# Kernel tuning notes

Hardware: AMD Instinct MI355X
Metric: run time of the kernel (lower is better)

## Reference

```python
import jax, jax.numpy as jnp
import numpy as np

B, M, FIN, FOUT, K, E = 4, 50000, 128, 128, 4, 800000


def setup_inputs() -> dict:
    key = jax.random.key(0)
    ks = jax.random.split(key, 8)
    x = jax.random.normal(ks[0], (B, M, FIN), dtype=jnp.float32)
    L_rows = jax.random.randint(ks[1], (E,), 0, M, dtype=jnp.int32)
    L_cols = jax.random.randint(ks[2], (E,), 0, M, dtype=jnp.int32)
    # stands in for the rescaled (0.75 * (2L/lmax - I)) Laplacian values
    L_vals = jax.random.normal(ks[3], (E,), dtype=jnp.float32) * 0.05
    stddev = 1.0 / np.sqrt(FIN * (K + 0.5) / 2.0)
    kernel = jax.random.normal(ks[4], (K * FIN, FOUT), dtype=jnp.float32) * stddev
    W_down = jax.random.normal(ks[5], (FOUT, FOUT // 8), dtype=jnp.float32) * (1.0 / np.sqrt(FOUT))
    b_down = jnp.zeros((FOUT // 8,), dtype=jnp.float32)
    W_up = jax.random.normal(ks[6], (FOUT // 8, FOUT), dtype=jnp.float32) * (1.0 / np.sqrt(FOUT // 8))
    b_up = jnp.zeros((FOUT,), dtype=jnp.float32)
    return {"x": x, "L_vals": L_vals, "L_rows": L_rows, "L_cols": L_cols,
            "kernel": kernel, "W_down": W_down, "b_down": b_down,
            "W_up": W_up, "b_up": b_up}


def reference(x, L_vals, L_rows, L_cols, kernel, W_down, b_down, W_up, b_up):
    B_, M_, Fin = x.shape
    K_ = kernel.shape[0] // Fin

    def spmm(X):  # sparse L [M,M] @ dense X [M, D]
        return jax.ops.segment_sum(L_vals[:, None] * X[L_cols], L_rows, num_segments=M_)

    # Chebyshev recurrence, operating on [M, Fin*B] like the TF code
    x0 = x.transpose(1, 2, 0).reshape(M_, Fin * B_)
    stack = [x0]
    if K_ > 1:
        x1 = spmm(x0)
        stack.append(x1)
    for _ in range(2, K_):
        x2 = 2.0 * spmm(x1) - x0
        stack.append(x2)
        x0, x1 = x1, x2

    # [K,M,Fin*B] -> [K,M,Fin,B] -> [B,M,Fin,K] -> [B*M, Fin*K]
    xs = jnp.stack(stack, axis=0).reshape(K_, M_, Fin, B_)
    xs = xs.transpose(3, 1, 2, 0).reshape(B_ * M_, Fin * K_)
    y = (xs @ kernel).reshape(B_, M_, -1)
    y = jax.nn.relu(y)

    # SE block: avg-pool over nodes, down (swish), up (sigmoid), scale
    s = jnp.mean(y, axis=1, keepdims=True)          # [B, 1, Fout]
    d = jax.nn.swish(s @ W_down + b_down)           # [B, 1, Fout/8]
    u = jax.nn.sigmoid(d @ W_up + b_up)             # [B, 1, Fout]
    return y * u
```

## Files before the change

kernel.cpp:

```cpp
#include <hip/hip_runtime.h>
#include <hip/hip_bf16.h>

#define BB 4
#define MM 50000
#define FINF 128
#define FOUTF 128
#define KCH 4
#define EE 800000
#define NROWS (BB*MM)
#define XC 512
#define CD 512

__device__ __forceinline__ float bf2f(unsigned short u){
    union{unsigned int i; float f;} v; v.i = ((unsigned int)u) << 16; return v.f;
}
__device__ __forceinline__ unsigned short f2bf(float f){
    union{float f; unsigned int i;} v; v.f = f;
    unsigned int r = v.i + 0x7FFF + ((v.i >> 16) & 1);
    return (unsigned short)(r >> 16);
}

typedef __bf16 bf16x8 __attribute__((ext_vector_type(8)));
typedef float  f32x4  __attribute__((ext_vector_type(4)));

__global__ __launch_bounds__(256) void k_init_x0(const float* __restrict__ x,
                                                 unsigned short* __restrict__ X0){
    int tid = blockIdx.x*256 + threadIdx.x;
    if (tid >= BB*MM*FINF/4) return;
    int f4 = tid & 31;
    int t  = tid >> 5;
    int m  = t % MM, b = t / MM;
    float4 v = ((const float4*)x)[tid];
    ushort4 o;
    o.x = f2bf(v.x); o.y = f2bf(v.y); o.z = f2bf(v.z); o.w = f2bf(v.w);
    *(ushort4*)(X0 + (size_t)m*XC + b*FINF + f4*4) = o;
}

__global__ __launch_bounds__(256) void k_prepw(const float* __restrict__ kern,
                                               unsigned short* __restrict__ Wt){
    int tid = blockIdx.x*256 + threadIdx.x;
    int c = tid & 511, n = tid >> 9;
    int kc = c >> 7, f = c & 127;
    int ns = n >> 4, l16 = n & 15;
    int ks = c >> 5, rem = c & 31, g = rem >> 3, j = rem & 7;
    int lane = g*16 + l16;
    Wt[((ns*16 + ks)*64 + lane)*8 + j] = f2bf(kern[(f*KCH + kc)*FOUTF + n]);
}

__global__ __launch_bounds__(256) void k_hist(const int* __restrict__ rows, int* __restrict__ counts){
    int e = blockIdx.x*256 + threadIdx.x;
    if (e < EE) atomicAdd(&counts[rows[e]], 1);
}

__global__ __launch_bounds__(1024) void k_scan(const int* __restrict__ counts,
                                               int* __restrict__ offs, int* __restrict__ cursor){
    __shared__ int part[1024];
    const int CH = (MM + 1023) / 1024;
    int t = threadIdx.x;
    int lo = t*CH; if (lo > MM) lo = MM;
    int hi = lo + CH; if (hi > MM) hi = MM;
    int s = 0;
    for (int i = lo; i < hi; ++i) s += counts[i];
    part[t] = s; __syncthreads();
    for (int d = 1; d < 1024; d <<= 1){
        int v = (t >= d) ? part[t-d] : 0;
        __syncthreads();
        part[t] += v;
        __syncthreads();
    }
    int run = (t == 0) ? 0 : part[t-1];
    for (int i = lo; i < hi; ++i){
        offs[i] = run; cursor[i] = run; run += counts[i];
    }
    if (t == 1023) offs[MM] = part[1023];
}

__global__ __launch_bounds__(256) void k_scatter(const int* __restrict__ rows, const int* __restrict__ cols,
                                                 const float* __restrict__ vals, int* __restrict__ cursor,
                                                 int* __restrict__ colv, float* __restrict__ valv){
    int e = blockIdx.x*256 + threadIdx.x;
    if (e >= EE) return;
    int r = rows[e];
    int pos = atomicAdd(&cursor[r], 1);
    colv[pos] = cols[e]; valv[pos] = vals[e];
}

__global__ __launch_bounds__(128) void k_spmm(const unsigned short* __restrict__ Xin,
                                              const unsigned short* __restrict__ Xprev,
                                              unsigned short* __restrict__ Xout,
                                              const int* __restrict__ offs,
                                              const int* __restrict__ colv,
                                              const float* __restrict__ valv,
                                              float alpha, int sub){
    int m = blockIdx.x, t = threadIdx.x;
    int c0 = t*4;
    int start = offs[m], end = offs[m+1];
    float a0=0.f, a1=0.f, a2=0.f, a3=0.f;

    int n  = end - start;
    int nb = n & ~3;
    int burst_end = start + nb;
    int j = start;

    int   cc[4];
    float vv[4];
    if (j < burst_end){
        #pragma unroll
        for (int q = 0; q < 4; ++q){ cc[q] = colv[j+q]; vv[q] = valv[j+q]; }
    }
    while (j < burst_end){
        int   c_[4];
        float v_[4];
        #pragma unroll
        for (int q = 0; q < 4; ++q){ c_[q] = cc[q]; v_[q] = vv[q]; }
        j += 4;
        if (j < burst_end){
            #pragma unroll
            for (int q = 0; q < 4; ++q){ cc[q] = colv[j+q]; vv[q] = valv[j+q]; }
        }
        ushort4 xv[4];
        #pragma unroll
        for (int q = 0; q < 4; ++q)
            xv[q] = *(const ushort4*)(Xin + (size_t)c_[q]*XC + c0);
        #pragma unroll
        for (int q = 0; q < 4; ++q){
            a0 += v_[q]*bf2f(xv[q].x); a1 += v_[q]*bf2f(xv[q].y);
            a2 += v_[q]*bf2f(xv[q].z); a3 += v_[q]*bf2f(xv[q].w);
        }
    }
    for (; j < end; ++j){
        int col = colv[j]; float val = valv[j];
        ushort4 xv = *(const ushort4*)(Xin + (size_t)col*XC + c0);
        a0 += val*bf2f(xv.x); a1 += val*bf2f(xv.y);
        a2 += val*bf2f(xv.z); a3 += val*bf2f(xv.w);
    }

    a0 *= alpha; a1 *= alpha; a2 *= alpha; a3 *= alpha;
    if (sub){
        ushort4 pv = *(const ushort4*)(Xprev + (size_t)m*XC + c0);
        a0 -= bf2f(pv.x); a1 -= bf2f(pv.y); a2 -= bf2f(pv.z); a3 -= bf2f(pv.w);
    }
    ushort4 o; o.x = f2bf(a0); o.y = f2bf(a1); o.z = f2bf(a2); o.w = f2bf(a3);
    *(ushort4*)(Xout + (size_t)m*XC + c0) = o;
}

__global__ __launch_bounds__(256, 2) void k_gemm(const unsigned short* __restrict__ X0,
                                                 const unsigned short* __restrict__ X1,
                                                 const unsigned short* __restrict__ X2,
                                                 const unsigned short* __restrict__ X3,
                                                 const unsigned short* __restrict__ Wt,
                                                 float* __restrict__ Y){
    const int wave = threadIdx.x >> 6;
    const int lane = threadIdx.x & 63;
    const int l16  = lane & 15;
    const int g    = lane >> 4;
    const int r0   = blockIdx.x*256 + wave*64;

    int aoff[4];
    #pragma unroll
    for (int i = 0; i < 4; ++i){
        int ra = r0 + i*16 + l16;
        if (ra >= NROWS) ra = NROWS-1;
        aoff[i] = (ra % MM)*XC + (ra / MM)*FINF + g*8;
    }

    const unsigned short* const Xs[4] = {X0, X1, X2, X3};

    f32x4 acc[4][8];
    #pragma unroll
    for (int i = 0; i < 4; ++i)
        #pragma unroll
        for (int j = 0; j < 8; ++j) acc[i][j] = (f32x4){0.f,0.f,0.f,0.f};

    bf16x8 a_cur[4], b_cur[8], a_nxt[4], b_nxt[8];

    {
        const unsigned short* Xb = Xs[0];
        #pragma unroll
        for (int i = 0; i < 4; ++i) a_cur[i] = *(const bf16x8*)(Xb + aoff[i]);
        #pragma unroll
        for (int ns = 0; ns < 8; ++ns) b_cur[ns] = *(const bf16x8*)(Wt + (ns*16)*512 + lane*8);
    }

    #pragma unroll
    for (int ks = 0; ks < 16; ++ks){
        if (ks < 15){
            const int kn = ks + 1;
            const unsigned short* Xb = Xs[kn >> 2];
            const int f0 = (kn & 3)*32;
            #pragma unroll
            for (int i = 0; i < 4; ++i) a_nxt[i] = *(const bf16x8*)(Xb + aoff[i] + f0);
            #pragma unroll
            for (int ns = 0; ns < 8; ++ns) b_nxt[ns] = *(const bf16x8*)(Wt + (ns*16 + kn)*512 + lane*8);
        }
        #pragma unroll
        for (int ns = 0; ns < 8; ++ns)
            #pragma unroll
            for (int i = 0; i < 4; ++i)
                acc[i][ns] = __builtin_amdgcn_mfma_f32_16x16x32_bf16(a_cur[i], b_cur[ns], acc[i][ns], 0, 0, 0);
        #pragma unroll
        for (int i = 0; i < 4; ++i) a_cur[i] = a_nxt[i];
        #pragma unroll
        for (int ns = 0; ns < 8; ++ns) b_cur[ns] = b_nxt[ns];
    }

    #pragma unroll
    for (int i = 0; i < 4; ++i){
        #pragma unroll
        for (int reg = 0; reg < 4; ++reg){
            int r = r0 + i*16 + g*4 + reg;
            if (r < NROWS){
                #pragma unroll
                for (int ns = 0; ns < 8; ++ns){
                    float v = acc[i][ns][reg];
                    Y[(size_t)r*FOUTF + ns*16 + l16] = v > 0.f ? v : 0.f;
                }
            }
        }
    }
}

__global__ __launch_bounds__(256) void k_colmean(const float* __restrict__ Y, float* __restrict__ sacc){
    int b = blockIdx.y, t = threadIdx.x;
    int c4 = t & 31, rs = t >> 5;
    const int rows = (MM + gridDim.x - 1) / gridDim.x;
    int m0 = blockIdx.x * rows;
    int mend = m0 + rows; if (mend > MM) mend = MM;
    float4 s = {0.f,0.f,0.f,0.f};
    for (int m = m0 + rs; m < mend; m += 8){
        float4 v = *(const float4*)(Y + ((size_t)b*MM + m)*FOUTF + c4*4);
        s.x += v.x; s.y += v.y; s.z += v.z; s.w += v.w;
    }
    __shared__ float4 red[8][32];
    red[rs][c4] = s;
    __syncthreads();
    if (t < 32){
        float4 a = red[0][t];
        #pragma unroll
        for (int i = 1; i < 8; ++i){
            float4 v = red[i][t];
            a.x += v.x; a.y += v.y; a.z += v.z; a.w += v.w;
        }
        atomicAdd(&sacc[b*FOUTF + t*4 + 0], a.x);
        atomicAdd(&sacc[b*FOUTF + t*4 + 1], a.y);
        atomicAdd(&sacc[b*FOUTF + t*4 + 2], a.z);
        atomicAdd(&sacc[b*FOUTF + t*4 + 3], a.w);
    }
}

__global__ __launch_bounds__(128) void k_se(const float* __restrict__ sacc,
                                            const float* __restrict__ Wd, const float* __restrict__ bd,
                                            const float* __restrict__ Wu, const float* __restrict__ bu,
                                            float* __restrict__ u){
    int b = blockIdx.x, t = threadIdx.x;
    __shared__ float sm[128];
    __shared__ float dsh[16];
    sm[t] = sacc[b*FOUTF + t] * (1.0f/MM);
    __syncthreads();
    if (t < 16){
        float a = bd[t];
        for (int f = 0; f < 128; ++f) a += sm[f]*Wd[f*16 + t];
        dsh[t] = a / (1.f + expf(-a));
    }
    __syncthreads();
    float a = bu[t];
    for (int j = 0; j < 16; ++j) a += dsh[j]*Wu[j*FOUTF + t];
    u[b*FOUTF + t] = 1.f/(1.f + expf(-a));
}

__global__ __launch_bounds__(256) void k_scale(const float* __restrict__ Y, const float* __restrict__ u,
                                               float* __restrict__ out){
    int tid = blockIdx.x*256 + threadIdx.x;
    if (tid >= NROWS*FOUTF/4) return;
    int b  = tid / (MM*FOUTF/4);
    int f4 = tid & 31;
    float4 yv = ((const float4*)Y)[tid];
    float4 uv = *(const float4*)(u + b*FOUTF + f4*4);
    float4 o;
    o.x = yv.x*uv.x; o.y = yv.y*uv.y; o.z = yv.z*uv.z; o.w = yv.w*uv.w;
    ((float4*)out)[tid] = o;
}

extern "C" void kernel_launch(void* const* d_in, const int* in_sizes, int n_in,
                              void* d_out, int out_size, void* d_ws, size_t ws_size,
                              hipStream_t stream){
    (void)in_sizes; (void)n_in; (void)out_size; (void)ws_size;
    const float* x    = (const float*)d_in[0];
    const float* lv   = (const float*)d_in[1];
    const int*   lr   = (const int*)d_in[2];
    const int*   lc   = (const int*)d_in[3];
    const float* kern = (const float*)d_in[4];
    const float* Wd   = (const float*)d_in[5];
    const float* bd   = (const float*)d_in[6];
    const float* Wu   = (const float*)d_in[7];
    const float* bu   = (const float*)d_in[8];
    float* out = (float*)d_out;

    char* w = (char*)d_ws;
    size_t off = 0;
    auto take = [&](size_t bytes)->char*{
        char* p = w + off; off += (bytes + 255) & ~(size_t)255; return p;
    };
    unsigned short* X[4];
    for (int i = 0; i < 4; ++i) X[i] = (unsigned short*)take((size_t)MM*XC*2);
    float* Y           = (float*)take((size_t)NROWS*FOUTF*4);
    unsigned short* Wt = (unsigned short*)take((size_t)FOUTF*CD*2);
    int* counts        = (int*)take((size_t)MM*4);
    int* offs          = (int*)take((size_t)(MM+1)*4);
    int* cursor        = (int*)take((size_t)MM*4);
    int* colv          = (int*)take((size_t)EE*4);
    float* valv        = (float*)take((size_t)EE*4);
    float* sacc        = (float*)take((size_t)BB*FOUTF*4);
    float* u           = (float*)take((size_t)BB*FOUTF*4);

    hipMemsetAsync(counts, 0, MM*4, stream);
    hipMemsetAsync(sacc, 0, BB*FOUTF*4, stream);

    k_init_x0<<<25000, 256, 0, stream>>>(x, X[0]);
    k_prepw<<<256, 256, 0, stream>>>(kern, Wt);
    k_hist<<<(EE+255)/256, 256, 0, stream>>>(lr, counts);
    k_scan<<<1, 1024, 0, stream>>>(counts, offs, cursor);
    k_scatter<<<(EE+255)/256, 256, 0, stream>>>(lr, lc, lv, cursor, colv, valv);

    k_spmm<<<MM, 128, 0, stream>>>(X[0], X[0], X[1], offs, colv, valv, 1.0f, 0);
    k_spmm<<<MM, 128, 0, stream>>>(X[1], X[0], X[2], offs, colv, valv, 2.0f, 1);
    k_spmm<<<MM, 128, 0, stream>>>(X[2], X[1], X[3], offs, colv, valv, 2.0f, 1);

    k_gemm<<<(NROWS+255)/256, 256, 0, stream>>>(X[0], X[1], X[2], X[3], Wt, Y);

    dim3 gmean(256, BB);
    k_colmean<<<gmean, 256, 0, stream>>>(Y, sacc);
    k_se<<<BB, 128, 0, stream>>>(sacc, Wd, bd, Wu, bu, u);
    k_scale<<<25000, 256, 0, stream>>>(Y, u, out);
}
```

Baseline: 907.4 us.

## Slab SpMM by column chunks, parallel scan, pack edges, fuse column mean into GEMM

The Chebyshev SpMM now runs in four column slabs of 128 channels, one wave per row, so each pass gathers from a smaller working set that fits better in cache. Column indices and values are packed into int2 edges. The single-block scan becomes a three-kernel multi-block scan. The SE column-sum is fused into the GEMM epilogue through shuffle and LDS reduction plus atomics, which removes the separate pass that re-read Y. The cost is twelve SpMM launches instead of three, each re-reading the edge list, plus more atomics where blocks straddle a batch boundary.

```diff
diff --git a/kernel.cpp b/kernel.cpp
--- a/kernel.cpp
+++ b/kernel.cpp
@@ -10,6 +10,10 @@
 #define NROWS (BB*MM)
 #define XC 512
 #define CD 512
+#define SLABS 4
+#define SC (XC/SLABS)
+#define SCB 512
+#define NSB ((MM + SCB - 1)/SCB)
 
 __device__ __forceinline__ float bf2f(unsigned short u){
     union{unsigned int i; float f;} v; v.i = ((unsigned int)u) << 16; return v.f;
@@ -52,96 +56,120 @@
     if (e < EE) atomicAdd(&counts[rows[e]], 1);
 }
 
-__global__ __launch_bounds__(1024) void k_scan(const int* __restrict__ counts,
+__global__ __launch_bounds__(256) void k_scanA(const int* __restrict__ counts, int* __restrict__ part){
+    __shared__ int red[256];
+    int b = blockIdx.x, t = threadIdx.x;
+    int i = b*SCB + t;
+    int s = 0;
+    if (i < MM) s += counts[i];
+    if (i + 256 < (b+1)*SCB && i + 256 < MM) s += counts[i+256];
+    red[t] = s; __syncthreads();
+    for (int d = 128; d > 0; d >>= 1){
+        if (t < d) red[t] += red[t+d];
+        __syncthreads();
+    }
+    if (t == 0) part[b] = red[0];
+}
+
+__global__ __launch_bounds__(128) void k_scanB(int* __restrict__ part){
+    __shared__ int sh[128];
+    int t = threadIdx.x;
+    sh[t] = (t < NSB) ? part[t] : 0;
+    __syncthreads();
+    for (int d = 1; d < 128; d <<= 1){
+        int v = (t >= d) ? sh[t-d] : 0;
+        __syncthreads();
+        sh[t] += v;
+        __syncthreads();
+    }
+    if (t < NSB) part[t] = sh[t];
+}
+
+__global__ __launch_bounds__(256) void k_scanC(const int* __restrict__ counts, const int* __restrict__ part,
                                                int* __restrict__ offs, int* __restrict__ cursor){
-    __shared__ int part[1024];
-    const int CH = (MM + 1023) / 1024;
-    int t = threadIdx.x;
-    int lo = t*CH; if (lo > MM) lo = MM;
-    int hi = lo + CH; if (hi > MM) hi = MM;
-    int s = 0;
-    for (int i = lo; i < hi; ++i) s += counts[i];
-    part[t] = s; __syncthreads();
-    for (int d = 1; d < 1024; d <<= 1){
-        int v = (t >= d) ? part[t-d] : 0;
-        __syncthreads();
-        part[t] += v;
-        __syncthreads();
-    }
-    int run = (t == 0) ? 0 : part[t-1];
-    for (int i = lo; i < hi; ++i){
-        offs[i] = run; cursor[i] = run; run += counts[i];
-    }
-    if (t == 1023) offs[MM] = part[1023];
+    __shared__ int sh[256];
+    int b = blockIdx.x, t = threadIdx.x;
+    int base = (b == 0) ? 0 : part[b-1];
+    int i0 = b*SCB + 2*t;
+    int c0 = (i0     < MM) ? counts[i0]   : 0;
+    int c1 = (i0 + 1 < MM) ? counts[i0+1] : 0;
+    sh[t] = c0 + c1; __syncthreads();
+    for (int d = 1; d < 256; d <<= 1){
+        int v = (t >= d) ? sh[t-d] : 0;
+        __syncthreads();
+        sh[t] += v;
+        __syncthreads();
+    }
+    int excl = base + sh[t] - (c0 + c1);
+    if (i0 < MM){ offs[i0] = excl;      cursor[i0] = excl; }
+    if (i0 + 1 < MM){ offs[i0+1] = excl + c0; cursor[i0+1] = excl + c0; }
+    if (b == gridDim.x-1 && t == 255) offs[MM] = EE;
 }
 
 __global__ __launch_bounds__(256) void k_scatter(const int* __restrict__ rows, const int* __restrict__ cols,
                                                  const float* __restrict__ vals, int* __restrict__ cursor,
-                                                 int* __restrict__ colv, float* __restrict__ valv){
+                                                 int2* __restrict__ edges){
     int e = blockIdx.x*256 + threadIdx.x;
     if (e >= EE) return;
     int r = rows[e];
     int pos = atomicAdd(&cursor[r], 1);
-    colv[pos] = cols[e]; valv[pos] = vals[e];
-}
-
-__global__ __launch_bounds__(128) void k_spmm(const unsigned short* __restrict__ Xin,
-                                              const unsigned short* __restrict__ Xprev,
-                                              unsigned short* __restrict__ Xout,
-                                              const int* __restrict__ offs,
-                                              const int* __restrict__ colv,
-                                              const float* __restrict__ valv,
-                                              float alpha, int sub){
-    int m = blockIdx.x, t = threadIdx.x;
-    int c0 = t*4;
+    edges[pos] = make_int2(cols[e], __float_as_int(vals[e]));
+}
+
+__global__ __launch_bounds__(256) void k_spmm_slab(const unsigned short* __restrict__ Xin,
+                                                   const unsigned short* __restrict__ Xprev,
+                                                   unsigned short* __restrict__ Xout,
+                                                   const int* __restrict__ offs,
+                                                   const int2* __restrict__ edges,
+                                                   float alpha, int sub, int cbase){
+    int m    = blockIdx.x*4 + (threadIdx.x >> 6);
+    int lane = threadIdx.x & 63;
+    size_t c0 = (size_t)cbase + lane*2;
     int start = offs[m], end = offs[m+1];
-    float a0=0.f, a1=0.f, a2=0.f, a3=0.f;
-
-    int n  = end - start;
-    int nb = n & ~3;
+    float a0 = 0.f, a1 = 0.f;
+
+    int nb = (end - start) & ~3;
     int burst_end = start + nb;
     int j = start;
 
-    int   cc[4];
-    float vv[4];
+    int2 ee[4];
     if (j < burst_end){
         #pragma unroll
-        for (int q = 0; q < 4; ++q){ cc[q] = colv[j+q]; vv[q] = valv[j+q]; }
+        for (int q = 0; q < 4; ++q) ee[q] = edges[j+q];
     }
     while (j < burst_end){
-        int   c_[4];
-        float v_[4];
-        #pragma unroll
-        for (int q = 0; q < 4; ++q){ c_[q] = cc[q]; v_[q] = vv[q]; }
+        int2 e_[4];
+        #pragma unroll
+        for (int q = 0; q < 4; ++q) e_[q] = ee[q];
         j += 4;
         if (j < burst_end){
             #pragma unroll
-            for (int q = 0; q < 4; ++q){ cc[q] = colv[j+q]; vv[q] = valv[j+q]; }
-        }
-        ushort4 xv[4];
+            for (int q = 0; q < 4; ++q) ee[q] = edges[j+q];
+        }
+        ushort2 xv[4];
         #pragma unroll
         for (int q = 0; q < 4; ++q)
-            xv[q] = *(const ushort4*)(Xin + (size_t)c_[q]*XC + c0);
+            xv[q] = *(const ushort2*)(Xin + (size_t)e_[q].x*XC + c0);
         #pragma unroll
         for (int q = 0; q < 4; ++q){
-            a0 += v_[q]*bf2f(xv[q].x); a1 += v_[q]*bf2f(xv[q].y);
-            a2 += v_[q]*bf2f(xv[q].z); a3 += v_[q]*bf2f(xv[q].w);
+            float val = __int_as_float(e_[q].y);
+            a0 += val*bf2f(xv[q].x); a1 += val*bf2f(xv[q].y);
         }
     }
     for (; j < end; ++j){
-        int col = colv[j]; float val = valv[j];
-        ushort4 xv = *(const ushort4*)(Xin + (size_t)col*XC + c0);
+        int2 e = edges[j];
+        float val = __int_as_float(e.y);
+        ushort2 xv = *(const ushort2*)(Xin + (size_t)e.x*XC + c0);
         a0 += val*bf2f(xv.x); a1 += val*bf2f(xv.y);
-        a2 += val*bf2f(xv.z); a3 += val*bf2f(xv.w);
-    }
-
-    a0 *= alpha; a1 *= alpha; a2 *= alpha; a3 *= alpha;
+    }
+
+    a0 *= alpha; a1 *= alpha;
     if (sub){
-        ushort4 pv = *(const ushort4*)(Xprev + (size_t)m*XC + c0);
-        a0 -= bf2f(pv.x); a1 -= bf2f(pv.y); a2 -= bf2f(pv.z); a3 -= bf2f(pv.w);
-    }
-    ushort4 o; o.x = f2bf(a0); o.y = f2bf(a1); o.z = f2bf(a2); o.w = f2bf(a3);
-    *(ushort4*)(Xout + (size_t)m*XC + c0) = o;
+        ushort2 pv = *(const ushort2*)(Xprev + (size_t)m*XC + c0);
+        a0 -= bf2f(pv.x); a1 -= bf2f(pv.y);
+    }
+    ushort2 o; o.x = f2bf(a0); o.y = f2bf(a1);
+    *(ushort2*)(Xout + (size_t)m*XC + c0) = o;
 }
 
 __global__ __launch_bounds__(256, 2) void k_gemm(const unsigned short* __restrict__ X0,
@@ -149,7 +177,8 @@
                                                  const unsigned short* __restrict__ X2,
                                                  const unsigned short* __restrict__ X3,
                                                  const unsigned short* __restrict__ Wt,
-                                                 float* __restrict__ Y){
+                                                 float* __restrict__ Y,
+                                                 float* __restrict__ sacc){
     const int wave = threadIdx.x >> 6;
     const int lane = threadIdx.x & 63;
     const int l16  = lane & 15;
@@ -203,6 +232,13 @@
         #pragma unroll
         for (int ns = 0; ns < 8; ++ns) b_cur[ns] = b_nxt[ns];
     }
+
+    __shared__ float ldsum[4][FOUTF];
+    const int rblk = blockIdx.x*256;
+    const bool fast = ((rblk / MM) == ((rblk + 255) / MM)) && (rblk + 255 < NROWS);
+    float csum[8];
+    #pragma unroll
+    for (int ns = 0; ns < 8; ++ns) csum[ns] = 0.f;
 
     #pragma unroll
     for (int i = 0; i < 4; ++i){
@@ -213,38 +249,33 @@
                 #pragma unroll
                 for (int ns = 0; ns < 8; ++ns){
                     float v = acc[i][ns][reg];
-                    Y[(size_t)r*FOUTF + ns*16 + l16] = v > 0.f ? v : 0.f;
+                    v = v > 0.f ? v : 0.f;
+                    Y[(size_t)r*FOUTF + ns*16 + l16] = v;
+                    if (fast) csum[ns] += v;
+                    else      atomicAdd(&sacc[(r/MM)*FOUTF + ns*16 + l16], v);
                 }
             }
         }
     }
-}
-
-__global__ __launch_bounds__(256) void k_colmean(const float* __restrict__ Y, float* __restrict__ sacc){
-    int b = blockIdx.y, t = threadIdx.x;
-    int c4 = t & 31, rs = t >> 5;
-    const int rows = (MM + gridDim.x - 1) / gridDim.x;
-    int m0 = blockIdx.x * rows;
-    int mend = m0 + rows; if (mend > MM) mend = MM;
-    float4 s = {0.f,0.f,0.f,0.f};
-    for (int m = m0 + rs; m < mend; m += 8){
-        float4 v = *(const float4*)(Y + ((size_t)b*MM + m)*FOUTF + c4*4);
-        s.x += v.x; s.y += v.y; s.z += v.z; s.w += v.w;
-    }
-    __shared__ float4 red[8][32];
-    red[rs][c4] = s;
-    __syncthreads();
-    if (t < 32){
-        float4 a = red[0][t];
-        #pragma unroll
-        for (int i = 1; i < 8; ++i){
-            float4 v = red[i][t];
-            a.x += v.x; a.y += v.y; a.z += v.z; a.w += v.w;
-        }
-        atomicAdd(&sacc[b*FOUTF + t*4 + 0], a.x);
-        atomicAdd(&sacc[b*FOUTF + t*4 + 1], a.y);
-        atomicAdd(&sacc[b*FOUTF + t*4 + 2], a.z);
-        atomicAdd(&sacc[b*FOUTF + t*4 + 3], a.w);
+    if (fast){
+        const int bidx = rblk / MM;
+        #pragma unroll
+        for (int ns = 0; ns < 8; ++ns){
+            float v = csum[ns];
+            v += __shfl_xor(v, 16);
+            v += __shfl_xor(v, 32);
+            csum[ns] = v;
+        }
+        if (lane < 16){
+            #pragma unroll
+            for (int ns = 0; ns < 8; ++ns) ldsum[wave][ns*16 + lane] = csum[ns];
+        }
+        __syncthreads();
+        int t = threadIdx.x;
+        if (t < FOUTF){
+            float s = ldsum[0][t] + ldsum[1][t] + ldsum[2][t] + ldsum[3][t];
+            atomicAdd(&sacc[bidx*FOUTF + t], s);
+        }
     }
 }
 
@@ -308,8 +339,8 @@
     int* counts        = (int*)take((size_t)MM*4);
     int* offs          = (int*)take((size_t)(MM+1)*4);
     int* cursor        = (int*)take((size_t)MM*4);
-    int* colv          = (int*)take((size_t)EE*4);
-    float* valv        = (float*)take((size_t)EE*4);
+    int2* edges        = (int2*)take((size_t)EE*8);
+    int* part          = (int*)take((size_t)NSB*4);
     float* sacc        = (float*)take((size_t)BB*FOUTF*4);
     float* u           = (float*)take((size_t)BB*FOUTF*4);
 
@@ -319,17 +350,20 @@
     k_init_x0<<<25000, 256, 0, stream>>>(x, X[0]);
     k_prepw<<<256, 256, 0, stream>>>(kern, Wt);
     k_hist<<<(EE+255)/256, 256, 0, stream>>>(lr, counts);
-    k_scan<<<1, 1024, 0, stream>>>(counts, offs, cursor);
-    k_scatter<<<(EE+255)/256, 256, 0, stream>>>(lr, lc, lv, cursor, colv, valv);
-
-    k_spmm<<<MM, 128, 0, stream>>>(X[0], X[0], X[1], offs, colv, valv, 1.0f, 0);
-    k_spmm<<<MM, 128, 0, stream>>>(X[1], X[0], X[2], offs, colv, valv, 2.0f, 1);
-    k_spmm<<<MM, 128, 0, stream>>>(X[2], X[1], X[3], offs, colv, valv, 2.0f, 1);
-
-    k_gemm<<<(NROWS+255)/256, 256, 0, stream>>>(X[0], X[1], X[2], X[3], Wt, Y);
-
-    dim3 gmean(256, BB);
-    k_colmean<<<gmean, 256, 0, stream>>>(Y, sacc);
+    k_scanA<<<NSB, 256, 0, stream>>>(counts, part);
+    k_scanB<<<1, 128, 0, stream>>>(part);
+    k_scanC<<<NSB, 256, 0, stream>>>(counts, part, offs, cursor);
+    k_scatter<<<(EE+255)/256, 256, 0, stream>>>(lr, lc, lv, cursor, edges);
+
+    for (int s = 0; s < SLABS; ++s){
+        int cbase = s*SC;
+        k_spmm_slab<<<MM/4, 256, 0, stream>>>(X[0], X[0], X[1], offs, edges, 1.0f, 0, cbase);
+        k_spmm_slab<<<MM/4, 256, 0, stream>>>(X[1], X[0], X[2], offs, edges, 2.0f, 1, cbase);
+        k_spmm_slab<<<MM/4, 256, 0, stream>>>(X[2], X[1], X[3], offs, edges, 2.0f, 1, cbase);
+    }
+
+    k_gemm<<<(NROWS+255)/256, 256, 0, stream>>>(X[0], X[1], X[2], X[3], Wt, Y, sacc);
+
     k_se<<<BB, 128, 0, stream>>>(sacc, Wd, bd, Wu, bu, u);
     k_scale<<<25000, 256, 0, stream>>>(Y, u, out);
 }
```

Result: faster. 857.6 us (-5.5%).
